# Kernel optimization log

Hardware: AMD Instinct MI355X
Metric: run time of the kernel (lower is better)

The kernel has to match this reference:

```python
import jax, jax.numpy as jnp
import numpy as np

B, I, O, G = 4096, 256, 256, 32


def setup_inputs() -> dict:
    key = jax.random.key(0)
    k1, k2, k3, k4 = jax.random.split(key, 4)
    x = jax.random.normal(k1, (B, I), dtype=jnp.float32)
    fouriercoeffs = jax.random.normal(k2, (2, O, I, G), dtype=jnp.float32) / (np.sqrt(I) * np.sqrt(G))
    bias = jnp.zeros((1, O), dtype=jnp.float32)
    mask = jnp.ones((I, O), dtype=jnp.float32)
    # scale_base = mu/sqrt(I) + sigma*(rand*2-1)/sqrt(I), mu=0, sigma=1
    scale_base = (jax.random.uniform(k3, (I, O), dtype=jnp.float32) * 2.0 - 1.0) / np.sqrt(I)
    scale_fft = jnp.ones((I, O), dtype=jnp.float32) * (1.0 / np.sqrt(I)) * mask
    return {"x": x, "fouriercoeffs": fouriercoeffs, "bias": bias, "mask": mask,
            "scale_base": scale_base, "scale_fft": scale_fft}


def reference(x, fouriercoeffs, bias, mask, scale_base, scale_fft):
    gridsize = fouriercoeffs.shape[-1]
    k = jnp.arange(1, gridsize + 1, dtype=x.dtype)          # (G,)
    kx = x[:, :, None] * k                                   # (B, I, G)
    c = jnp.cos(kx)
    s = jnp.sin(kx)
    # einsum 'dbik,djik->bij' with d=2 split into cos/sin parts
    y = jnp.einsum('bik,jik->bij', c, fouriercoeffs[0]) \
        + jnp.einsum('bik,jik->bij', s, fouriercoeffs[1])    # (B, I, O)
    base = jax.nn.silu(x)                                     # SiLU base branch
    y = scale_base[None, :, :] * base[:, :, None] + scale_fft[None, :, :] * y
    y = (mask[None, :, :] * y).sum(axis=1)                    # sum over inputdim -> (B, O)
    y = y + bias
    return y
```

## Files before the change

### kernel.cpp

```cpp
#include <hip/hip_runtime.h>
#include <stdint.h>


#define I_DIM 256
#define O_DIM 256
#define G_DIM 32
#define B_DIM 4096

#define BM 128
#define BN 128
#define KSPLIT 16
#define ICH 16
#define PITCH 72

typedef short s8v __attribute__((ext_vector_type(8)));
typedef float f4v __attribute__((ext_vector_type(4)));

__device__ __forceinline__ uint32_t pack2bf16(float a, float b) {
  uint32_t ua = __builtin_bit_cast(uint32_t, a);
  uint32_t ub = __builtin_bit_cast(uint32_t, b);
  ua += 0x7FFFu + ((ua >> 16) & 1u);
  ub += 0x7FFFu + ((ub >> 16) & 1u);
  return (ua >> 16) | (ub & 0xFFFF0000u);
}
__device__ __forceinline__ unsigned short bf16_rne(float a) {
  uint32_t ua = __builtin_bit_cast(uint32_t, a);
  ua += 0x7FFFu + ((ua >> 16) & 1u);
  return (unsigned short)(ua >> 16);
}
__device__ __forceinline__ uint32_t cvtpk_bf16(float a, float b) {
  uint32_t r;
  asm("v_cvt_pk_bf16_f32 %0, %1, %2" : "=v"(r) : "v"(a), "v"(b));
  return r;
}
__device__ __forceinline__ float silu_f(float v) { return v / (1.0f + __expf(-v)); }

__device__ __forceinline__ void gen_feat(float xv, int half, uint32_t* fb) {
  float s, c;
  __sincosf(xv, &s, &c);
  const float m2 = 2.f * c;
  float f0 = half ? s : c;
  float f1 = m2 * f0 - (half ? 0.f : 1.f);
  fb[0] = cvtpk_bf16(f0, f1);
  #pragma unroll
  for (int p = 1; p < 16; ++p) {
    float f2 = m2 * f1 - f0;
    float f3 = m2 * f2 - f1;
    fb[p] = cvtpk_bf16(f2, f3);
    f0 = f2; f1 = f3;
  }
}

__global__ __launch_bounds__(256) void prep_bs_kernel(
    const float* __restrict__ fc, const float* __restrict__ mask,
    const float* __restrict__ sfft, short* __restrict__ Bp)
{
  const int gid = blockIdx.x * 256 + threadIdx.x;
  const int h = gid & 1;
  const int d = (gid >> 1) & 1;
  const int p = gid >> 2;
  const int i = p >> 8, j = p & 255;
  const size_t ij = (size_t)i * O_DIM + j;
  const float sf = sfft[ij] * mask[ij];
  const float* src = fc + (size_t)d * (O_DIM * I_DIM * G_DIM)
                        + ((size_t)j * I_DIM + i) * G_DIM + h * 16;
  uint32_t w[8];
  #pragma unroll
  for (int q = 0; q < 4; ++q) {
    float4 v = ((const float4*)src)[q];
    w[2*q]   = pack2bf16(v.x * sf, v.y * sf);
    w[2*q+1] = pack2bf16(v.z * sf, v.w * sf);
  }
  uint4* dst = (uint4*)(Bp + (size_t)p * 64);
  const int xr = j & 7;
  #pragma unroll
  for (int c = 0; c < 2; ++c)
    dst[(4 * d + 2 * h + c) ^ xr] = make_uint4(w[4*c], w[4*c+1], w[4*c+2], w[4*c+3]);
}

__global__ __launch_bounds__(256, 4) void kan_main5(
    const float* __restrict__ x,
    const short* __restrict__ Bp,
    const float* __restrict__ mask,
    const float* __restrict__ scale_base,
    unsigned short* __restrict__ partial)
{
  __shared__ short A_lds[BM * 64];
  __shared__ short B_lds[BN * 64];

  const int tid = threadIdx.x;
  const int bx  = blockIdx.x;
  const int kc  = bx & 15;
  const int bn  = (bx >> 4) & 1;
  const int bm  = bx >> 5;
  const int i0  = kc * ICH;

  const int lane = tid & 63;
  const int wave = tid >> 6;
  const int wm   = wave & 1;
  const int wn   = wave >> 1;
  const int l15  = lane & 15;
  const int quad = lane >> 4;

  f4v acc[4][4];
  #pragma unroll
  for (int a = 0; a < 4; ++a)
    #pragma unroll
    for (int b = 0; b < 4; ++b)
      acc[a][b] = (f4v){0.f, 0.f, 0.f, 0.f};

  const int row  = tid >> 1;
  const int half = tid & 1;
  const int mg   = bm * BM + row;
  const int jg   = bn * BN + row;
  const int xr   = row & 7;

  const float* xrow = x + (size_t)mg * I_DIM + i0;
  uint4* Arow = (uint4*)&A_lds[row * 64];
  const int c0 = half * 4;
  const int q0 = wave * 4;
  const size_t dma_lane_off = (size_t)lane * 8;

  uint32_t aNext[16];
  gen_feat(xrow[0], half, aNext);
  float xnxt = xrow[1];

  for (int it = 0; it < ICH; ++it) {
    __syncthreads();

    Arow[(c0 + 0) ^ xr] = make_uint4(aNext[0],  aNext[1],  aNext[2],  aNext[3]);
    Arow[(c0 + 1) ^ xr] = make_uint4(aNext[4],  aNext[5],  aNext[6],  aNext[7]);
    Arow[(c0 + 2) ^ xr] = make_uint4(aNext[8],  aNext[9],  aNext[10], aNext[11]);
    Arow[(c0 + 3) ^ xr] = make_uint4(aNext[12], aNext[13], aNext[14], aNext[15]);

    {
      const size_t rbase = ((size_t)(i0 + it) * 256 + bn * BN) * 64;
      #pragma unroll
      for (int c = 0; c < 4; ++c) {
        const int q = q0 + c;
        const short* g = Bp + rbase + (size_t)q * 8 * 64 + dma_lane_off;
        __builtin_amdgcn_global_load_lds(
            (const __attribute__((address_space(1))) void*)g,
            (__attribute__((address_space(3))) void*)&B_lds[q * 8 * 64],
            16, 0, 0);
      }
    }

    if (it + 1 < ICH) {
      gen_feat(xnxt, half, aNext);
      if (it + 2 < ICH) xnxt = xrow[it + 2];
    }

    __syncthreads();

    __builtin_amdgcn_s_setprio(1);
    #pragma unroll
    for (int ks = 0; ks < 2; ++ks) {
      s8v a[4], b[4];
      #pragma unroll
      for (int tm = 0; tm < 4; ++tm) {
        const int r = wm * 64 + tm * 16 + l15;
        a[tm] = *(const s8v*)&A_lds[r * 64 + (((ks * 4 + quad) ^ (r & 7)) * 8)];
      }
      #pragma unroll
      for (int tn = 0; tn < 4; ++tn) {
        const int r = wn * 64 + tn * 16 + l15;
        b[tn] = *(const s8v*)&B_lds[r * 64 + (((ks * 4 + quad) ^ (r & 7)) * 8)];
      }
      #pragma unroll
      for (int tm = 0; tm < 4; ++tm)
        #pragma unroll
        for (int tn = 0; tn < 4; ++tn)
          acc[tm][tn] = __builtin_amdgcn_mfma_f32_16x16x32_bf16(a[tm], b[tn], acc[tm][tn], 0, 0, 0);
    }
    __builtin_amdgcn_s_setprio(0);
  }

  __syncthreads();
  {
    const float* xb = xrow + half * 8;
    float4 v0 = ((const float4*)xb)[0];
    float4 v1 = ((const float4*)xb)[1];
    uint32_t a0 = pack2bf16(silu_f(v0.x), silu_f(v0.y));
    uint32_t a1 = pack2bf16(silu_f(v0.z), silu_f(v0.w));
    uint32_t a2 = pack2bf16(silu_f(v1.x), silu_f(v1.y));
    uint32_t a3 = pack2bf16(silu_f(v1.z), silu_f(v1.w));
    Arow[half ^ xr]       = make_uint4(a0, a1, a2, a3);
    Arow[(2 + half) ^ xr] = make_uint4(0, 0, 0, 0);

    uint32_t w[4];
    #pragma unroll
    for (int p = 0; p < 4; ++p) {
      const int ia = i0 + half * 8 + 2 * p;
      const size_t o0 = (size_t)ia * O_DIM + jg;
      const size_t o1 = o0 + O_DIM;
      w[p] = pack2bf16(scale_base[o0] * mask[o0], scale_base[o1] * mask[o1]);
    }
    uint4* Brow = (uint4*)&B_lds[row * 64];
    Brow[half ^ xr]       = make_uint4(w[0], w[1], w[2], w[3]);
    Brow[(2 + half) ^ xr] = make_uint4(0, 0, 0, 0);
  }
  __syncthreads();
  {
    __builtin_amdgcn_s_setprio(1);
    s8v a[4], b[4];
    #pragma unroll
    for (int tm = 0; tm < 4; ++tm) {
      const int r = wm * 64 + tm * 16 + l15;
      a[tm] = *(const s8v*)&A_lds[r * 64 + ((quad ^ (r & 7)) * 8)];
    }
    #pragma unroll
    for (int tn = 0; tn < 4; ++tn) {
      const int r = wn * 64 + tn * 16 + l15;
      b[tn] = *(const s8v*)&B_lds[r * 64 + ((quad ^ (r & 7)) * 8)];
    }
    #pragma unroll
    for (int tm = 0; tm < 4; ++tm)
      #pragma unroll
      for (int tn = 0; tn < 4; ++tn)
        acc[tm][tn] = __builtin_amdgcn_mfma_f32_16x16x32_bf16(a[tm], b[tn], acc[tm][tn], 0, 0, 0);
    __builtin_amdgcn_s_setprio(0);
  }

  unsigned short* pbase = partial + (size_t)kc * B_DIM * O_DIM;
  #pragma unroll
  for (int tm = 0; tm < 4; ++tm) {
    #pragma unroll
    for (int tn = 0; tn < 4; ++tn) {
      const int n_g = bn * BN + wn * 64 + tn * 16 + l15;
      f4v v = acc[tm][tn];
      #pragma unroll
      for (int r = 0; r < 4; ++r) {
        const int m_g = bm * BM + wm * 64 + tm * 16 + quad * 4 + r;
        pbase[(size_t)m_g * O_DIM + n_g] = bf16_rne(v[r]);
      }
    }
  }
}

__global__ __launch_bounds__(256) void reduce_kernel(
    const unsigned short* __restrict__ partial, const float* __restrict__ bias,
    float* __restrict__ out)
{
  const int g  = blockIdx.x * 256 + threadIdx.x;
  const int m  = g >> 5;
  const int n8 = (g & 31) << 3;
  const unsigned short* p = partial + (size_t)m * O_DIM + n8;

  float acc[8];
  {
    float4 b0 = ((const float4*)(bias + n8))[0];
    float4 b1 = ((const float4*)(bias + n8))[1];
    acc[0] = b0.x; acc[1] = b0.y; acc[2] = b0.z; acc[3] = b0.w;
    acc[4] = b1.x; acc[5] = b1.y; acc[6] = b1.z; acc[7] = b1.w;
  }
  #pragma unroll
  for (int kc = 0; kc < KSPLIT; ++kc) {
    const uint4 v = *(const uint4*)(p + (size_t)kc * (B_DIM * O_DIM));
    acc[0] += __builtin_bit_cast(float, v.x << 16);
    acc[1] += __builtin_bit_cast(float, v.x & 0xFFFF0000u);
    acc[2] += __builtin_bit_cast(float, v.y << 16);
    acc[3] += __builtin_bit_cast(float, v.y & 0xFFFF0000u);
    acc[4] += __builtin_bit_cast(float, v.z << 16);
    acc[5] += __builtin_bit_cast(float, v.z & 0xFFFF0000u);
    acc[6] += __builtin_bit_cast(float, v.w << 16);
    acc[7] += __builtin_bit_cast(float, v.w & 0xFFFF0000u);
  }
  float* o = out + (size_t)m * O_DIM + n8;
  ((float4*)o)[0] = make_float4(acc[0], acc[1], acc[2], acc[3]);
  ((float4*)o)[1] = make_float4(acc[4], acc[5], acc[6], acc[7]);
}

__global__ __launch_bounds__(256, 4) void kan_fft_fallback(
    const float* __restrict__ x, const float* __restrict__ fc,
    const float* __restrict__ bias, const float* __restrict__ mask,
    const float* __restrict__ scale_base, const float* __restrict__ scale_fft,
    float* __restrict__ out)
{
  __shared__ short A_lds[BM * PITCH];
  __shared__ short B_lds[BN * PITCH];

  const int tid = threadIdx.x;
  const int bx  = blockIdx.x;
  const int kc  = bx & 15;
  const int bn  = (bx >> 4) & 1;
  const int bm  = bx >> 5;
  const int i0  = kc * ICH;

  const int lane = tid & 63;
  const int wave = tid >> 6;
  const int wm   = wave & 1;
  const int wn   = wave >> 1;
  const int l15  = lane & 15;
  const int kgrp = (lane >> 4) * 8;

  f4v acc[4][4];
  #pragma unroll
  for (int a = 0; a < 4; ++a)
    #pragma unroll
    for (int b = 0; b < 4; ++b)
      acc[a][b] = (f4v){0.f, 0.f, 0.f, 0.f};

  const int row  = tid >> 1;
  const int half = tid & 1;
  const int mg   = bm * BM + row;
  const int jg   = bn * BN + row;

  const float* xrow   = x + (size_t)mg * I_DIM + i0;
  const float* fcbase = fc + (size_t)half * (O_DIM * I_DIM * G_DIM)
                           + ((size_t)jg * I_DIM + i0) * G_DIM;
  uint32_t* Arow = (uint32_t*)&A_lds[row * PITCH + half * 32];
  uint32_t* Brow = (uint32_t*)&B_lds[row * PITCH + half * 32];

  for (int it = 0; it < ICH; ++it) {
    __syncthreads();
    {
      uint32_t fb[16];
      gen_feat(xrow[it], half, fb);
      ((uint4*)Arow)[0] = make_uint4(fb[0],  fb[1],  fb[2],  fb[3]);
      ((uint4*)Arow)[1] = make_uint4(fb[4],  fb[5],  fb[6],  fb[7]);
      ((uint4*)Arow)[2] = make_uint4(fb[8],  fb[9],  fb[10], fb[11]);
      ((uint4*)Arow)[3] = make_uint4(fb[12], fb[13], fb[14], fb[15]);
    }
    {
      const int i = i0 + it;
      const size_t ij = (size_t)i * O_DIM + jg;
      const float sf  = scale_fft[ij] * mask[ij];
      const float* src = fcbase + it * G_DIM;
      uint32_t wb[16];
      #pragma unroll
      for (int q = 0; q < 8; ++q) {
        float4 v = ((const float4*)src)[q];
        wb[2*q]   = pack2bf16(v.x * sf, v.y * sf);
        wb[2*q+1] = pack2bf16(v.z * sf, v.w * sf);
      }
      ((uint4*)Brow)[0] = make_uint4(wb[0],  wb[1],  wb[2],  wb[3]);
      ((uint4*)Brow)[1] = make_uint4(wb[4],  wb[5],  wb[6],  wb[7]);
      ((uint4*)Brow)[2] = make_uint4(wb[8],  wb[9],  wb[10], wb[11]);
      ((uint4*)Brow)[3] = make_uint4(wb[12], wb[13], wb[14], wb[15]);
    }
    __syncthreads();
    #pragma unroll
    for (int ks = 0; ks < 2; ++ks) {
      s8v a[4], b[4];
      #pragma unroll
      for (int tm = 0; tm < 4; ++tm)
        a[tm] = *(const s8v*)&A_lds[(wm * 64 + tm * 16 + l15) * PITCH + ks * 32 + kgrp];
      #pragma unroll
      for (int tn = 0; tn < 4; ++tn)
        b[tn] = *(const s8v*)&B_lds[(wn * 64 + tn * 16 + l15) * PITCH + ks * 32 + kgrp];
      #pragma unroll
      for (int tm = 0; tm < 4; ++tm)
        #pragma unroll
        for (int tn = 0; tn < 4; ++tn)
          acc[tm][tn] = __builtin_amdgcn_mfma_f32_16x16x32_bf16(a[tm], b[tn], acc[tm][tn], 0, 0, 0);
    }
  }

  __syncthreads();
  {
    const float* xb = xrow + half * 8;
    float4 v0 = ((const float4*)xb)[0];
    float4 v1 = ((const float4*)xb)[1];
    uint32_t a0 = pack2bf16(silu_f(v0.x), silu_f(v0.y));
    uint32_t a1 = pack2bf16(silu_f(v0.z), silu_f(v0.w));
    uint32_t a2 = pack2bf16(silu_f(v1.x), silu_f(v1.y));
    uint32_t a3 = pack2bf16(silu_f(v1.z), silu_f(v1.w));
    ((uint4*)&A_lds[row * PITCH + half * 8])[0]      = make_uint4(a0, a1, a2, a3);
    ((uint4*)&A_lds[row * PITCH + 16 + half * 8])[0] = make_uint4(0, 0, 0, 0);
    uint32_t w[4];
    #pragma unroll
    for (int p = 0; p < 4; ++p) {
      const int ia = i0 + half * 8 + 2 * p;
      const size_t o0 = (size_t)ia * O_DIM + jg;
      const size_t o1 = o0 + O_DIM;
      w[p] = pack2bf16(scale_base[o0] * mask[o0], scale_base[o1] * mask[o1]);
    }
    ((uint4*)&B_lds[row * PITCH + half * 8])[0]      = make_uint4(w[0], w[1], w[2], w[3]);
    ((uint4*)&B_lds[row * PITCH + 16 + half * 8])[0] = make_uint4(0, 0, 0, 0);
  }
  __syncthreads();
  {
    s8v a[4], b[4];
    #pragma unroll
    for (int tm = 0; tm < 4; ++tm)
      a[tm] = *(const s8v*)&A_lds[(wm * 64 + tm * 16 + l15) * PITCH + kgrp];
    #pragma unroll
    for (int tn = 0; tn < 4; ++tn)
      b[tn] = *(const s8v*)&B_lds[(wn * 64 + tn * 16 + l15) * PITCH + kgrp];
    #pragma unroll
    for (int tm = 0; tm < 4; ++tm)
      #pragma unroll
      for (int tn = 0; tn < 4; ++tn)
        acc[tm][tn] = __builtin_amdgcn_mfma_f32_16x16x32_bf16(a[tm], b[tn], acc[tm][tn], 0, 0, 0);
  }

  const int quad = lane >> 4;
  #pragma unroll
  for (int tm = 0; tm < 4; ++tm) {
    #pragma unroll
    for (int tn = 0; tn < 4; ++tn) {
      const int n_g = bn * BN + wn * 64 + tn * 16 + l15;
      f4v v = acc[tm][tn];
      #pragma unroll
      for (int r = 0; r < 4; ++r) {
        const int m_g = bm * BM + wm * 64 + tm * 16 + quad * 4 + r;
        float val = v[r];
        if (kc == 0) val += bias[n_g];
        atomicAdd(&out[(size_t)m_g * O_DIM + n_g], val);
      }
    }
  }
}

extern "C" void kernel_launch(void* const* d_in, const int* in_sizes, int n_in,
                              void* d_out, int out_size, void* d_ws, size_t ws_size,
                              hipStream_t stream) {
  const float* x          = (const float*)d_in[0];
  const float* fc         = (const float*)d_in[1];
  const float* bias       = (const float*)d_in[2];
  const float* mask       = (const float*)d_in[3];
  const float* scale_base = (const float*)d_in[4];
  const float* scale_fft  = (const float*)d_in[5];
  float* out = (float*)d_out;

  const size_t BP_B    = (size_t)I_DIM * O_DIM * 64 * 2;
  const size_t PARTH_B = (size_t)KSPLIT * B_DIM * O_DIM * 2;

  if (ws_size >= BP_B + PARTH_B) {
    short*          Bp      = (short*)d_ws;
    unsigned short* partial = (unsigned short*)((char*)d_ws + BP_B);
    prep_bs_kernel<<<dim3(1024), dim3(256), 0, stream>>>(fc, mask, scale_fft, Bp);
    kan_main5<<<dim3(1024), dim3(256), 0, stream>>>(x, Bp, mask, scale_base, partial);
    reduce_kernel<<<dim3(512), dim3(256), 0, stream>>>(partial, bias, out);
  } else {
    hipMemsetAsync(d_out, 0, (size_t)out_size * sizeof(float), stream);
    kan_fft_fallback<<<dim3(1024), dim3(256), 0, stream>>>(
        x, fc, bias, mask, scale_base, scale_fft, out);
  }
}
```

Before: 121.9 us.

## Load B fragments directly from global in MFMA layout and double-buffer A

The prep kernel now writes the Fourier coefficient matrix pre-arranged in MFMA operand fragment order, so the main kernel loads B operands straight from global memory into registers instead of staging them through LDS with global_load_lds. The A feature tile is double-buffered in LDS, which drops one __syncthreads per iteration and lets the next chunk's feature generation overlap the current MFMAs. In exchange, B reads now go directly through the cache hierarchy per wave with no LDS sharing between the two waves that use the same B columns, and register pressure rises from holding eight B fragments.

```diff
diff --git a/kernel.cpp b/kernel.cpp
--- a/kernel.cpp
+++ b/kernel.cpp
@@ -56,14 +56,15 @@
     const float* __restrict__ sfft, short* __restrict__ Bp)
 {
   const int gid = blockIdx.x * 256 + threadIdx.x;
-  const int h = gid & 1;
-  const int d = (gid >> 1) & 1;
+  const int e = gid & 3;
   const int p = gid >> 2;
   const int i = p >> 8, j = p & 255;
+  const int d = e >> 1;
+  const int koff = (e & 1) * 16;
   const size_t ij = (size_t)i * O_DIM + j;
   const float sf = sfft[ij] * mask[ij];
-  const float* src = fc + (size_t)d * (O_DIM * I_DIM * G_DIM)
-                        + ((size_t)j * I_DIM + i) * G_DIM + h * 16;
+  const float* src = fc + ((size_t)d * (O_DIM * I_DIM)
+                          + (size_t)j * I_DIM + i) * G_DIM + koff;
   uint32_t w[8];
   #pragma unroll
   for (int q = 0; q < 4; ++q) {
@@ -71,22 +72,21 @@
     w[2*q]   = pack2bf16(v.x * sf, v.y * sf);
     w[2*q+1] = pack2bf16(v.z * sf, v.w * sf);
   }
-  uint4* dst = (uint4*)(Bp + (size_t)p * 64);
-  const int xr = j & 7;
-  #pragma unroll
-  for (int c = 0; c < 2; ++c)
-    dst[(4 * d + 2 * h + c) ^ xr] = make_uint4(w[4*c], w[4*c+1], w[4*c+2], w[4*c+3]);
-}
-
-__global__ __launch_bounds__(256, 4) void kan_main5(
+  const int h = j >> 6, r = j & 63;
+  const int cb = d * 4 + (e & 1) * 2;
+  short* dst = Bp + ((size_t)i * 4 + h) * 4096;
+  *(uint4*)&dst[(cb * 64 + r) * 8]       = make_uint4(w[0], w[1], w[2], w[3]);
+  *(uint4*)&dst[((cb + 1) * 64 + r) * 8] = make_uint4(w[4], w[5], w[6], w[7]);
+}
+
+__global__ __launch_bounds__(256, 4) void kan_main6(
     const float* __restrict__ x,
     const short* __restrict__ Bp,
     const float* __restrict__ mask,
     const float* __restrict__ scale_base,
     unsigned short* __restrict__ partial)
 {
-  __shared__ short A_lds[BM * 64];
-  __shared__ short B_lds[BN * 64];
+  __shared__ short A_lds[2][BM * 64];
 
   const int tid = threadIdx.x;
   const int bx  = blockIdx.x;
@@ -116,62 +116,60 @@
   const int xr   = row & 7;
 
   const float* xrow = x + (size_t)mg * I_DIM + i0;
-  uint4* Arow = (uint4*)&A_lds[row * 64];
   const int c0 = half * 4;
-  const int q0 = wave * 4;
-  const size_t dma_lane_off = (size_t)lane * 8;
-
-  uint32_t aNext[16];
-  gen_feat(xrow[0], half, aNext);
+
+  const short* bbase = Bp + ((size_t)i0 * 4 + (size_t)(bn * 2 + wn)) * 4096;
+
+  {
+    uint32_t fb[16];
+    gen_feat(xrow[0], half, fb);
+    uint4* Ar = (uint4*)&A_lds[0][row * 64];
+    Ar[(c0 + 0) ^ xr] = make_uint4(fb[0],  fb[1],  fb[2],  fb[3]);
+    Ar[(c0 + 1) ^ xr] = make_uint4(fb[4],  fb[5],  fb[6],  fb[7]);
+    Ar[(c0 + 2) ^ xr] = make_uint4(fb[8],  fb[9],  fb[10], fb[11]);
+    Ar[(c0 + 3) ^ xr] = make_uint4(fb[12], fb[13], fb[14], fb[15]);
+  }
   float xnxt = xrow[1];
 
   for (int it = 0; it < ICH; ++it) {
     __syncthreads();
 
-    Arow[(c0 + 0) ^ xr] = make_uint4(aNext[0],  aNext[1],  aNext[2],  aNext[3]);
-    Arow[(c0 + 1) ^ xr] = make_uint4(aNext[4],  aNext[5],  aNext[6],  aNext[7]);
-    Arow[(c0 + 2) ^ xr] = make_uint4(aNext[8],  aNext[9],  aNext[10], aNext[11]);
-    Arow[(c0 + 3) ^ xr] = make_uint4(aNext[12], aNext[13], aNext[14], aNext[15]);
-
+    s8v b[2][4];
     {
-      const size_t rbase = ((size_t)(i0 + it) * 256 + bn * BN) * 64;
-      #pragma unroll
-      for (int c = 0; c < 4; ++c) {
-        const int q = q0 + c;
-        const short* g = Bp + rbase + (size_t)q * 8 * 64 + dma_lane_off;
-        __builtin_amdgcn_global_load_lds(
-            (const __attribute__((address_space(1))) void*)g,
-            (__attribute__((address_space(3))) void*)&B_lds[q * 8 * 64],
-            16, 0, 0);
-      }
+      const short* bsl = bbase + (size_t)it * 16384;
+      #pragma unroll
+      for (int ks = 0; ks < 2; ++ks)
+        #pragma unroll
+        for (int tn = 0; tn < 4; ++tn)
+          b[ks][tn] = *(const s8v*)&bsl[((ks * 4 + quad) * 64 + tn * 16 + l15) * 8];
     }
 
     if (it + 1 < ICH) {
-      gen_feat(xnxt, half, aNext);
+      uint32_t fb[16];
+      gen_feat(xnxt, half, fb);
+      uint4* Ar = (uint4*)&A_lds[(it + 1) & 1][row * 64];
+      Ar[(c0 + 0) ^ xr] = make_uint4(fb[0],  fb[1],  fb[2],  fb[3]);
+      Ar[(c0 + 1) ^ xr] = make_uint4(fb[4],  fb[5],  fb[6],  fb[7]);
+      Ar[(c0 + 2) ^ xr] = make_uint4(fb[8],  fb[9],  fb[10], fb[11]);
+      Ar[(c0 + 3) ^ xr] = make_uint4(fb[12], fb[13], fb[14], fb[15]);
       if (it + 2 < ICH) xnxt = xrow[it + 2];
     }
 
-    __syncthreads();
-
+    const short* Ac = &A_lds[it & 1][0];
     __builtin_amdgcn_s_setprio(1);
     #pragma unroll
     for (int ks = 0; ks < 2; ++ks) {
-      s8v a[4], b[4];
+      s8v a[4];
       #pragma unroll
       for (int tm = 0; tm < 4; ++tm) {
         const int r = wm * 64 + tm * 16 + l15;
-        a[tm] = *(const s8v*)&A_lds[r * 64 + (((ks * 4 + quad) ^ (r & 7)) * 8)];
-      }
-      #pragma unroll
-      for (int tn = 0; tn < 4; ++tn) {
-        const int r = wn * 64 + tn * 16 + l15;
-        b[tn] = *(const s8v*)&B_lds[r * 64 + (((ks * 4 + quad) ^ (r & 7)) * 8)];
+        a[tm] = *(const s8v*)&Ac[r * 64 + (((ks * 4 + quad) ^ (r & 7)) * 8)];
       }
       #pragma unroll
       for (int tm = 0; tm < 4; ++tm)
         #pragma unroll
         for (int tn = 0; tn < 4; ++tn)
-          acc[tm][tn] = __builtin_amdgcn_mfma_f32_16x16x32_bf16(a[tm], b[tn], acc[tm][tn], 0, 0, 0);
+          acc[tm][tn] = __builtin_amdgcn_mfma_f32_16x16x32_bf16(a[tm], b[ks][tn], acc[tm][tn], 0, 0, 0);
     }
     __builtin_amdgcn_s_setprio(0);
   }
@@ -185,6 +183,7 @@
     uint32_t a1 = pack2bf16(silu_f(v0.z), silu_f(v0.w));
     uint32_t a2 = pack2bf16(silu_f(v1.x), silu_f(v1.y));
     uint32_t a3 = pack2bf16(silu_f(v1.z), silu_f(v1.w));
+    uint4* Arow = (uint4*)&A_lds[0][row * 64];
     Arow[half ^ xr]       = make_uint4(a0, a1, a2, a3);
     Arow[(2 + half) ^ xr] = make_uint4(0, 0, 0, 0);
 
@@ -196,7 +195,7 @@
       const size_t o1 = o0 + O_DIM;
       w[p] = pack2bf16(scale_base[o0] * mask[o0], scale_base[o1] * mask[o1]);
     }
-    uint4* Brow = (uint4*)&B_lds[row * 64];
+    uint4* Brow = (uint4*)&A_lds[1][row * 64];
     Brow[half ^ xr]       = make_uint4(w[0], w[1], w[2], w[3]);
     Brow[(2 + half) ^ xr] = make_uint4(0, 0, 0, 0);
   }
@@ -207,12 +206,12 @@
     #pragma unroll
     for (int tm = 0; tm < 4; ++tm) {
       const int r = wm * 64 + tm * 16 + l15;
-      a[tm] = *(const s8v*)&A_lds[r * 64 + ((quad ^ (r & 7)) * 8)];
+      a[tm] = *(const s8v*)&A_lds[0][r * 64 + ((quad ^ (r & 7)) * 8)];
     }
     #pragma unroll
     for (int tn = 0; tn < 4; ++tn) {
       const int r = wn * 64 + tn * 16 + l15;
-      b[tn] = *(const s8v*)&B_lds[r * 64 + ((quad ^ (r & 7)) * 8)];
+      b[tn] = *(const s8v*)&A_lds[1][r * 64 + ((quad ^ (r & 7)) * 8)];
     }
     #pragma unroll
     for (int tm = 0; tm < 4; ++tm)
@@ -431,7 +430,7 @@
     short*          Bp      = (short*)d_ws;
     unsigned short* partial = (unsigned short*)((char*)d_ws + BP_B);
     prep_bs_kernel<<<dim3(1024), dim3(256), 0, stream>>>(fc, mask, scale_fft, Bp);
-    kan_main5<<<dim3(1024), dim3(256), 0, stream>>>(x, Bp, mask, scale_base, partial);
+    kan_main6<<<dim3(1024), dim3(256), 0, stream>>>(x, Bp, mask, scale_base, partial);
     reduce_kernel<<<dim3(512), dim3(256), 0, stream>>>(partial, bias, out);
   } else {
     hipMemsetAsync(d_out, 0, (size_t)out_size * sizeof(float), stream);
```

New measurement: 154.7 us. 1.27x slower.
